# Kernel tuning notes

Measured on AMD Instinct MI355X. Metric: run time of the kernel, lower is better.

Reference implementation:

```python
import jax, jax.numpy as jnp
import numpy as np

B, CIN, H, W = 16, 1, 256, 256
WIDTH = 64
MODES = 32
LAYERS = 4
COUT = 1


def conv1x1(x, w, b):
    # x: [B,Ci,H,W], w: [Co,Ci], b: [Co]
    return jnp.einsum('bixy,oi->boxy', x, w) + b[None, :, None, None]


def mlp(x, w1, b1, w2, b2):
    # Conv2d(ci,mid,1) -> GELU(exact) -> Conv2d(mid,co,1)
    return conv1x1(jax.nn.gelu(conv1x1(x, w1, b1), approximate=False), w2, b2)


def spectral_conv2d(x, w1r, w1i, w2r, w2i):
    # x: [B,C,H,W]; weights: [Ci,Co,m1,m2] (real/imag parts of cfloat params)
    b, c, h, w = x.shape
    m1, m2 = w1r.shape[2], w1r.shape[3]
    co = w1r.shape[1]
    x_ft = jnp.fft.rfft2(x)  # [B,C,H,W//2+1] complex64
    w1 = w1r + 1j * w1i
    w2 = w2r + 1j * w2i
    top = jnp.einsum('bixy,ioxy->boxy', x_ft[:, :, :m1, :m2], w1)
    bot = jnp.einsum('bixy,ioxy->boxy', x_ft[:, :, -m1:, :m2], w2)
    out_ft = jnp.zeros((b, co, h, w // 2 + 1), dtype=x_ft.dtype)
    out_ft = out_ft.at[:, :, :m1, :m2].set(top).at[:, :, -m1:, :m2].set(bot)
    return jnp.fft.irfft2(out_ft, s=(h, w))


def setup_inputs() -> dict:
    key = jax.random.key(0)
    ks = iter(jax.random.split(key, 32))
    scale = 1.0 / (WIDTH * WIDTH)
    f32 = jnp.float32
    inp = {}
    inp['x'] = jax.random.normal(next(ks), (B, CIN, H, W), dtype=f32)
    # lifting 1x1 conv
    inp['p_w'] = jax.random.normal(next(ks), (WIDTH, CIN), dtype=f32) / np.sqrt(CIN)
    inp['p_b'] = jnp.zeros((WIDTH,), dtype=f32)
    # per-layer spectral weights (real/imag of uniform cfloat init)
    shp = (LAYERS, WIDTH, WIDTH, MODES, MODES)
    inp['sw1r'] = scale * jax.random.uniform(next(ks), shp, dtype=f32)
    inp['sw1i'] = scale * jax.random.uniform(next(ks), shp, dtype=f32)
    inp['sw2r'] = scale * jax.random.uniform(next(ks), shp, dtype=f32)
    inp['sw2i'] = scale * jax.random.uniform(next(ks), shp, dtype=f32)
    # per-layer channel MLP (mid_channels = WIDTH)
    inp['m1w'] = jax.random.normal(next(ks), (LAYERS, WIDTH, WIDTH), dtype=f32) / np.sqrt(WIDTH)
    inp['m1b'] = jnp.zeros((LAYERS, WIDTH), dtype=f32)
    inp['m2w'] = jax.random.normal(next(ks), (LAYERS, WIDTH, WIDTH), dtype=f32) / np.sqrt(WIDTH)
    inp['m2b'] = jnp.zeros((LAYERS, WIDTH), dtype=f32)
    # per-layer skip 1x1 conv
    inp['skw'] = jax.random.normal(next(ks), (LAYERS, WIDTH, WIDTH), dtype=f32) / np.sqrt(WIDTH)
    inp['skb'] = jnp.zeros((LAYERS, WIDTH), dtype=f32)
    # projection MLP (mid = 4*WIDTH)
    inp['q1w'] = jax.random.normal(next(ks), (4 * WIDTH, WIDTH), dtype=f32) / np.sqrt(WIDTH)
    inp['q1b'] = jnp.zeros((4 * WIDTH,), dtype=f32)
    inp['q2w'] = jax.random.normal(next(ks), (COUT, 4 * WIDTH), dtype=f32) / np.sqrt(4 * WIDTH)
    inp['q2b'] = jnp.zeros((COUT,), dtype=f32)
    return inp


def reference(x, p_w, p_b, sw1r, sw1i, sw2r, sw2i, m1w, m1b, m2w, m2b,
              skw, skb, q1w, q1b, q2w, q2b):
    h = conv1x1(x, p_w, p_b)  # lift to [B,WIDTH,H,W]
    for l in range(LAYERS):
        x1 = spectral_conv2d(h, sw1r[l], sw1i[l], sw2r[l], sw2i[l])
        x1 = mlp(x1, m1w[l], m1b[l], m2w[l], m2b[l])
        x2 = conv1x1(h, skw[l], skb[l])
        h = x1 + x2
        if l < LAYERS - 1:
            h = jax.nn.gelu(h, approximate=False)
    return mlp(h, q1w, q1b, q2w, q2b)  # [B,COUT,H,W]
```

## Files before the change

### kernel.cpp

```cpp
#include <hip/hip_runtime.h>
#include <math.h>

#define NC 64
#define NH 256
#define NW 256
#define NM 32
#define NKY 64
#define HW 65536

typedef short bfrag __attribute__((ext_vector_type(8)));
typedef float facc  __attribute__((ext_vector_type(4)));
#define MFMA(a,b,c) __builtin_amdgcn_mfma_f32_16x16x32_bf16(a,b,c,0,0,0)

static constexpr float PI_F = 3.14159265358979323846f;

__device__ __forceinline__ unsigned short f2b(float f) {
  unsigned b = __float_as_uint(f);
  return (unsigned short)((b + 0x7FFFu + ((b >> 16) & 1u)) >> 16);
}
__device__ __forceinline__ float b2f(unsigned short h) {
  return __uint_as_float((unsigned)h << 16);
}

__device__ __forceinline__ float gelu_f(float x) {
  float z = fabsf(x) * 0.70710678118654752f;
  float t = 1.0f / (1.0f + 0.3275911f * z);
  float e = __expf(-z * z);
  float p = t * (0.254829592f + t * (-0.284496736f + t * (1.421413741f +
            t * (-1.453152027f + t * 1.061405429f))));
  float er = copysignf(1.0f - p * e, x);
  return 0.5f * x * (1.0f + er);
}

__global__ void k_tEy(unsigned short* __restrict__ eh, unsigned short* __restrict__ el) {
  int i = blockIdx.x * 256 + threadIdx.x;
  int m = i >> 8, y = i & 255;
  int kyi = m & 63;
  int ky = (kyi < 32) ? kyi : (192 + kyi);
  int a = (ky * y) & 255;
  float s, c; sincosf((float)a * (PI_F / 128.f), &s, &c);
  float v = (m < 64) ? c : -s;
  unsigned short h = f2b(v);
  eh[i] = h; el[i] = f2b(v - b2f(h));
}
__global__ void k_tEx(unsigned short* __restrict__ eh, unsigned short* __restrict__ el) {
  int i = blockIdx.x * 256 + threadIdx.x;
  int m = i >> 9, k = i & 511;
  int x = k & 255, plane = k >> 8, kx = m & 31;
  int a = (kx * x) & 255;
  float s, c; sincosf((float)a * (PI_F / 128.f), &s, &c);
  float v = (m < 32) ? (plane ? s : c) : (plane ? c : -s);
  unsigned short h = f2b(v);
  eh[i] = h; el[i] = f2b(v - b2f(h));
}
__global__ void k_tWy(unsigned short* __restrict__ eh, unsigned short* __restrict__ el) {
  int i = blockIdx.x * 256 + threadIdx.x;
  int row = i >> 7, k = i & 127;
  int y = row & 255, part = row >> 8;
  int kyi = k & 63, plane = k >> 6;
  int ky = (kyi < 32) ? kyi : (192 + kyi);
  int a = (ky * y) & 255;
  float s, c; sincosf((float)a * (PI_F / 128.f), &s, &c);
  float v = (part == 0) ? (plane ? -s : c) : (plane ? c : s);
  unsigned short h = f2b(v);
  eh[i] = h; el[i] = f2b(v - b2f(h));
}
__global__ void k_tCx(unsigned short* __restrict__ eh, unsigned short* __restrict__ el) {
  int i = blockIdx.x * 256 + threadIdx.x;
  int x = i >> 6, k = i & 63;
  int kx = k & 31, plane = k >> 5;
  float w = ((kx == 0) ? 1.0f : 2.0f) / 65536.0f;
  int a = (kx * x) & 255;
  float s, c; sincosf((float)a * (PI_F / 128.f), &s, &c);
  float v = plane ? (-w * s) : (w * c);
  unsigned short h = f2b(v);
  eh[i] = h; el[i] = f2b(v - b2f(h));
}

__global__ void k_cvt2(const float* __restrict__ src, unsigned short* __restrict__ hi,
                       unsigned short* __restrict__ lo, int n) {
  int i = blockIdx.x * 256 + threadIdx.x;
  if (i < n) {
    float v = src[i];
    unsigned short h = f2b(v);
    hi[i] = h;
    lo[i] = f2b(v - b2f(h));
  }
}

__global__ __launch_bounds__(256) void k_lift(const float* __restrict__ x,
                                              const float* __restrict__ pw,
                                              const float* __restrict__ pb,
                                              unsigned short* __restrict__ hh,
                                              unsigned short* __restrict__ hl) {
  int b = blockIdx.y;
  int yx = blockIdx.x * 256 + threadIdx.x;
  float v = x[(size_t)b * HW + yx];
  size_t o = (size_t)b * NC * HW + yx;
  for (int c = 0; c < NC; ++c) {
    float u = v * pw[c] + pb[c];
    unsigned short hi = f2b(u);
    hh[o + (size_t)c * HW] = hi;
    hl[o + (size_t)c * HW] = f2b(u - b2f(hi));
  }
}

__global__ __launch_bounds__(256) void k_fy2(const unsigned short* __restrict__ hh,
                                             const unsigned short* __restrict__ hl,
                                             const unsigned short* __restrict__ Ah,
                                             const unsigned short* __restrict__ Al,
                                             float* __restrict__ Xc, int Ncol) {
  int tid = threadIdx.x, wv = tid >> 6, ln = tid & 63, g16 = ln >> 4, l15 = ln & 15;
  int colbase = blockIdx.x * 128 + wv * 32;
  facc acc[8][2];
#pragma unroll
  for (int mf = 0; mf < 8; ++mf)
#pragma unroll
    for (int pf = 0; pf < 2; ++pf) acc[mf][pf] = (facc)0.f;
#pragma unroll 1
  for (int ks = 0; ks < 8; ++ks) {
    int kof = g16 * 8 + 32 * ks;
    bfrag bh[2], bl[2];
#pragma unroll
    for (int pf = 0; pf < 2; ++pf) {
      int col = colbase + pf * 16 + l15;
      size_t o = (size_t)(col >> 8) * HW + (col & 255) + (size_t)kof * 256;
#pragma unroll
      for (int j = 0; j < 8; ++j) {
        bh[pf][j] = (short)hh[o + j * 256];
        bl[pf][j] = (short)hl[o + j * 256];
      }
    }
#pragma unroll
    for (int mf = 0; mf < 8; ++mf) {
      int row = 16 * mf + l15;
      bfrag ah = *(const bfrag*)(Ah + row * 256 + kof);
      bfrag al = *(const bfrag*)(Al + row * 256 + kof);
#pragma unroll
      for (int pf = 0; pf < 2; ++pf) {
        acc[mf][pf] = MFMA(ah, bh[pf], acc[mf][pf]);
        acc[mf][pf] = MFMA(ah, bl[pf], acc[mf][pf]);
        acc[mf][pf] = MFMA(al, bh[pf], acc[mf][pf]);
      }
    }
  }
#pragma unroll
  for (int mf = 0; mf < 8; ++mf)
#pragma unroll
    for (int pf = 0; pf < 2; ++pf) {
      int col = colbase + pf * 16 + l15;
#pragma unroll
      for (int r = 0; r < 4; ++r)
        Xc[(size_t)(16 * mf + 4 * g16 + r) * Ncol + col] = acc[mf][pf][r];
    }
}

__global__ __launch_bounds__(256) void k_fx2(const float* __restrict__ Xc,
                                             const unsigned short* __restrict__ Ah,
                                             const unsigned short* __restrict__ Al,
                                             float* __restrict__ X2r,
                                             float* __restrict__ X2i, int NcXc) {
  int tid = threadIdx.x, wv = tid >> 6, ln = tid & 63, g16 = ln >> 4, l15 = ln & 15;
  int colbase = blockIdx.x * 64 + wv * 16;
  facc acc[4];
#pragma unroll
  for (int mf = 0; mf < 4; ++mf) acc[mf] = (facc)0.f;
#pragma unroll 1
  for (int ks = 0; ks < 16; ++ks) {
    int plane = ks >> 3;
    int x0 = (ks & 7) * 32 + g16 * 8;
    int kof = g16 * 8 + 32 * ks;
    bfrag bh, bl;
    {
      int col = colbase + l15;
      const float* p = Xc + (size_t)(plane * 64 + (col & 63)) * NcXc + (col >> 6) * 256 + x0;
      float4 u0 = *(const float4*)p;
      float4 u1 = *(const float4*)(p + 4);
      float tv[8] = {u0.x, u0.y, u0.z, u0.w, u1.x, u1.y, u1.z, u1.w};
#pragma unroll
      for (int j = 0; j < 8; ++j) {
        unsigned short hi = f2b(tv[j]);
        bh[j] = (short)hi;
        bl[j] = (short)f2b(tv[j] - b2f(hi));
      }
    }
#pragma unroll
    for (int mf = 0; mf < 4; ++mf) {
      int row = 16 * mf + l15;
      bfrag ah = *(const bfrag*)(Ah + row * 512 + kof);
      bfrag al = *(const bfrag*)(Al + row * 512 + kof);
      acc[mf] = MFMA(ah, bh, acc[mf]);
      acc[mf] = MFMA(ah, bl, acc[mf]);
      acc[mf] = MFMA(al, bh, acc[mf]);
    }
  }
#pragma unroll
  for (int mf = 0; mf < 4; ++mf) {
    int col = colbase + l15;
    float* base = (mf >= 2) ? X2i : X2r;
    int kxb = 16 * (mf & 1) + 4 * g16;
    float4 v = make_float4(acc[mf][0], acc[mf][1], acc[mf][2], acc[mf][3]);
    *(float4*)(base + (size_t)col * 32 + kxb) = v;
  }
}

__global__ __launch_bounds__(512) void k_spec(const float* __restrict__ X2r,
                                              const float* __restrict__ X2i,
                                              const float* __restrict__ w1r,
                                              const float* __restrict__ w1i,
                                              const float* __restrict__ w2r,
                                              const float* __restrict__ w2i,
                                              float* __restrict__ S, int Ncs) {
  int b = blockIdx.y;
  int och = blockIdx.x & 3;
  int kyi = blockIdx.x >> 2;
  __shared__ float2 xs[NC * NM];
  for (int idx = threadIdx.x; idx < NC * NM; idx += 512) {
    int i = idx >> 5, kx = idx & 31;
    size_t c2 = ((size_t)(b * 64 + i) * 64 + kyi) * 32 + kx;
    xs[idx] = make_float2(X2r[c2], X2i[c2]);
  }
  __syncthreads();
  int kx = threadIdx.x & 31;
  int ol = threadIdx.x >> 5;
  int o = och * 16 + ol;
  int kym = kyi & 31;
  const float* wr = (kyi < 32) ? w1r : w2r;
  const float* wi = (kyi < 32) ? w1i : w2i;
  size_t wb = ((size_t)o * NM + kym) * NM + kx;
  float ar = 0.f, ai = 0.f;
#pragma unroll 4
  for (int i = 0; i < NC; ++i) {
    float2 xv = xs[i * NM + kx];
    float wrv = wr[wb + (size_t)i * 65536];
    float wiv = wi[wb + (size_t)i * 65536];
    ar += xv.x * wrv - xv.y * wiv;
    ai += xv.x * wiv + xv.y * wrv;
  }
  size_t cco = (size_t)(b * 64 + o) * 32 + kx;
  S[(size_t)kyi * Ncs + cco] = ar;
  S[(size_t)(64 + kyi) * Ncs + cco] = ai;
}

__global__ __launch_bounds__(256) void k_iy2(const float* __restrict__ S,
                                             const unsigned short* __restrict__ Ah,
                                             const unsigned short* __restrict__ Al,
                                             float* __restrict__ t2, int Ncs) {
  int tid = threadIdx.x, wv = tid >> 6, ln = tid & 63, g16 = ln >> 4, l15 = ln & 15;
  int colbase = blockIdx.x * 128 + wv * 32;
  int rowb = blockIdx.y * 64;
  facc acc[4][2];
#pragma unroll
  for (int mf = 0; mf < 4; ++mf)
#pragma unroll
    for (int pf = 0; pf < 2; ++pf) acc[mf][pf] = (facc)0.f;
#pragma unroll 1
  for (int ks = 0; ks < 4; ++ks) {
    int kof = g16 * 8 + 32 * ks;
    bfrag bh[2], bl[2];
#pragma unroll
    for (int pf = 0; pf < 2; ++pf) {
      int col = colbase + pf * 16 + l15;
      const float* p = S + (size_t)kof * Ncs + col;
#pragma unroll
      for (int j = 0; j < 8; ++j) {
        float v = p[(size_t)j * Ncs];
        unsigned short hi = f2b(v);
        bh[pf][j] = (short)hi;
        bl[pf][j] = (short)f2b(v - b2f(hi));
      }
    }
#pragma unroll
    for (int mf = 0; mf < 4; ++mf) {
      int row = rowb + 16 * mf + l15;
      bfrag ah = *(const bfrag*)(Ah + row * 128 + kof);
      bfrag al = *(const bfrag*)(Al + row * 128 + kof);
#pragma unroll
      for (int pf = 0; pf < 2; ++pf) {
        acc[mf][pf] = MFMA(ah, bh[pf], acc[mf][pf]);
        acc[mf][pf] = MFMA(ah, bl[pf], acc[mf][pf]);
        acc[mf][pf] = MFMA(al, bh[pf], acc[mf][pf]);
      }
    }
  }
#pragma unroll
  for (int mf = 0; mf < 4; ++mf)
#pragma unroll
    for (int pf = 0; pf < 2; ++pf) {
      int col = colbase + pf * 16 + l15;
#pragma unroll
      for (int r = 0; r < 4; ++r)
        t2[(size_t)(rowb + 16 * mf + 4 * g16 + r) * Ncs + col] = acc[mf][pf][r];
    }
}

__global__ __launch_bounds__(256) void k_ix2(const float* __restrict__ t2,
                                             const unsigned short* __restrict__ Ah,
                                             const unsigned short* __restrict__ Al,
                                             unsigned short* __restrict__ x1h,
                                             unsigned short* __restrict__ x1l, int Nct) {
  int tid = threadIdx.x, wv = tid >> 6, ln = tid & 63, g16 = ln >> 4, l15 = ln & 15;
  int colbase = blockIdx.x * 128 + wv * 32;
  int rowb = blockIdx.y * 128;
  facc acc[8][2];
#pragma unroll
  for (int mf = 0; mf < 8; ++mf)
#pragma unroll
    for (int pf = 0; pf < 2; ++pf) acc[mf][pf] = (facc)0.f;
#pragma unroll 1
  for (int ks = 0; ks < 2; ++ks) {
    int kof = g16 * 8 + 32 * ks;
    bfrag bh[2], bl[2];
#pragma unroll
    for (int pf = 0; pf < 2; ++pf) {
      int col = colbase + pf * 16 + l15;
      const float* p = t2 + (size_t)(ks * 256 + (col & 255)) * Nct + (col >> 8) * 32 + g16 * 8;
      float4 u0 = *(const float4*)p;
      float4 u1 = *(const float4*)(p + 4);
      float tv[8] = {u0.x, u0.y, u0.z, u0.w, u1.x, u1.y, u1.z, u1.w};
#pragma unroll
      for (int j = 0; j < 8; ++j) {
        unsigned short hi = f2b(tv[j]);
        bh[pf][j] = (short)hi;
        bl[pf][j] = (short)f2b(tv[j] - b2f(hi));
      }
    }
#pragma unroll
    for (int mf = 0; mf < 8; ++mf) {
      int row = rowb + 16 * mf + l15;
      bfrag ah = *(const bfrag*)(Ah + row * 64 + kof);
      bfrag al = *(const bfrag*)(Al + row * 64 + kof);
#pragma unroll
      for (int pf = 0; pf < 2; ++pf) {
        acc[mf][pf] = MFMA(ah, bh[pf], acc[mf][pf]);
        acc[mf][pf] = MFMA(ah, bl[pf], acc[mf][pf]);
        acc[mf][pf] = MFMA(al, bh[pf], acc[mf][pf]);
      }
    }
  }
#pragma unroll
  for (int mf = 0; mf < 8; ++mf)
#pragma unroll
    for (int pf = 0; pf < 2; ++pf) {
      int col = colbase + pf * 16 + l15;
      int bc = col >> 8, y = col & 255;
      int xb = rowb + 16 * mf + 4 * g16;
      ushort4 hv, lv;
#pragma unroll
      for (int r = 0; r < 4; ++r) {
        float v = acc[mf][pf][r];
        unsigned short hi = f2b(v);
        ((unsigned short*)&hv)[r] = hi;
        ((unsigned short*)&lv)[r] = f2b(v - b2f(hi));
      }
      size_t o = (size_t)bc * HW + y * 256 + xb;
      *(ushort4*)(x1h + o) = hv;
      *(ushort4*)(x1l + o) = lv;
    }
}

__global__ __launch_bounds__(256) void k_mlp1s(unsigned short* __restrict__ x1h,
                                               unsigned short* __restrict__ x1l,
                                               const unsigned short* __restrict__ w1h,
                                               const unsigned short* __restrict__ w1l,
                                               const float* __restrict__ b1p) {
  __shared__ unsigned short whs[64 * 72], wls[64 * 72];
  int tid = threadIdx.x;
  for (int i = tid; i < 64 * 64; i += 256) {
    int r = i >> 6, c = i & 63;
    whs[r * 72 + c] = w1h[i];
    wls[r * 72 + c] = w1l[i];
  }
  int wv = tid >> 6, ln = tid & 63, g16 = ln >> 4, l15 = ln & 15;
  int b = blockIdx.y;
  unsigned short* xh = x1h + (size_t)b * NC * HW;
  unsigned short* xl = x1l + (size_t)b * NC * HW;
  float b1v[4][4];
#pragma unroll
  for (int mf = 0; mf < 4; ++mf)
#pragma unroll
    for (int r = 0; r < 4; ++r) b1v[mf][r] = b1p[16 * mf + 4 * g16 + r];
  __syncthreads();
  for (int t = 0; t < 4; ++t) {
    int pxb = (blockIdx.x * 4 + t) * 128 + wv * 32;
    facc a1[4][2];
#pragma unroll
    for (int mf = 0; mf < 4; ++mf)
#pragma unroll
      for (int pf = 0; pf < 2; ++pf) {
        facc z; z[0] = b1v[mf][0]; z[1] = b1v[mf][1]; z[2] = b1v[mf][2]; z[3] = b1v[mf][3];
        a1[mf][pf] = z;
      }
#pragma unroll
    for (int ks = 0; ks < 2; ++ks) {
      bfrag xhb[2], xlb[2];
#pragma unroll
      for (int pf = 0; pf < 2; ++pf) {
        int px = pxb + pf * 16 + l15;
#pragma unroll
        for (int j = 0; j < 8; ++j) {
          int c = g16 * 8 + j + 32 * ks;
          xhb[pf][j] = (short)xh[(size_t)c * HW + px];
          xlb[pf][j] = (short)xl[(size_t)c * HW + px];
        }
      }
#pragma unroll
      for (int mf = 0; mf < 4; ++mf) {
        bfrag wh = *(const bfrag*)(whs + (16 * mf + l15) * 72 + g16 * 8 + 32 * ks);
        bfrag wl = *(const bfrag*)(wls + (16 * mf + l15) * 72 + g16 * 8 + 32 * ks);
#pragma unroll
        for (int pf = 0; pf < 2; ++pf) {
          a1[mf][pf] = MFMA(wh, xhb[pf], a1[mf][pf]);
          a1[mf][pf] = MFMA(wh, xlb[pf], a1[mf][pf]);
          a1[mf][pf] = MFMA(wl, xhb[pf], a1[mf][pf]);
        }
      }
    }
#pragma unroll
    for (int mf = 0; mf < 4; ++mf)
#pragma unroll
      for (int pf = 0; pf < 2; ++pf) {
        int px = pxb + pf * 16 + l15;
#pragma unroll
        for (int r = 0; r < 4; ++r) {
          float v = gelu_f(a1[mf][pf][r]);
          unsigned short hi = f2b(v);
          size_t idx = (size_t)(16 * mf + 4 * g16 + r) * HW + px;
          xh[idx] = hi;
          xl[idx] = f2b(v - b2f(hi));
        }
      }
  }
}

__global__ __launch_bounds__(256) void k_mix2(const unsigned short* __restrict__ midh,
                                              const unsigned short* __restrict__ midl,
                                              unsigned short* __restrict__ hh_,
                                              unsigned short* __restrict__ hl_,
                                              const unsigned short* __restrict__ w2h,
                                              const unsigned short* __restrict__ w2l,
                                              const unsigned short* __restrict__ skh,
                                              const unsigned short* __restrict__ skl,
                                              const float* __restrict__ b2p,
                                              const float* __restrict__ skbp,
                                              int do_gelu) {
  __shared__ unsigned short w2hs[64 * 72], w2ls[64 * 72], skhs[64 * 72], skls[64 * 72];
  int tid = threadIdx.x;
  for (int i = tid; i < 64 * 64; i += 256) {
    int r = i >> 6, c = i & 63;
    w2hs[r * 72 + c] = w2h[i];
    w2ls[r * 72 + c] = w2l[i];
    skhs[r * 72 + c] = skh[i];
    skls[r * 72 + c] = skl[i];
  }
  int wv = tid >> 6, ln = tid & 63, g16 = ln >> 4, l15 = ln & 15;
  int b = blockIdx.y;
  const unsigned short* mh = midh + (size_t)b * NC * HW;
  const unsigned short* ml = midl + (size_t)b * NC * HW;
  unsigned short* hbh = hh_ + (size_t)b * NC * HW;
  unsigned short* hbl = hl_ + (size_t)b * NC * HW;
  float b2v[4][4];
#pragma unroll
  for (int mf = 0; mf < 4; ++mf)
#pragma unroll
    for (int r = 0; r < 4; ++r) {
      int o = 16 * mf + 4 * g16 + r;
      b2v[mf][r] = b2p[o] + skbp[o];
    }
  __syncthreads();
  for (int t = 0; t < 4; ++t) {
    int pxb = (blockIdx.x * 4 + t) * 128 + wv * 32;
    facc a2[4][2];
#pragma unroll
    for (int mf = 0; mf < 4; ++mf)
#pragma unroll
      for (int pf = 0; pf < 2; ++pf) {
        facc z; z[0] = b2v[mf][0]; z[1] = b2v[mf][1]; z[2] = b2v[mf][2]; z[3] = b2v[mf][3];
        a2[mf][pf] = z;
      }
#pragma unroll
    for (int ks = 0; ks < 2; ++ks) {
      bfrag mhb[2], mlb[2], hhb[2], hlb[2];
#pragma unroll
      for (int pf = 0; pf < 2; ++pf) {
        int px = pxb + pf * 16 + l15;
#pragma unroll
        for (int j = 0; j < 8; ++j) {
          int c = g16 * 8 + j + 32 * ks;
          mhb[pf][j] = (short)mh[(size_t)c * HW + px];
          mlb[pf][j] = (short)ml[(size_t)c * HW + px];
          hhb[pf][j] = (short)hbh[(size_t)c * HW + px];
          hlb[pf][j] = (short)hbl[(size_t)c * HW + px];
        }
      }
#pragma unroll
      for (int mf = 0; mf < 4; ++mf) {
        bfrag w2hf = *(const bfrag*)(w2hs + (16 * mf + l15) * 72 + g16 * 8 + 32 * ks);
        bfrag w2lf = *(const bfrag*)(w2ls + (16 * mf + l15) * 72 + g16 * 8 + 32 * ks);
        bfrag skhf = *(const bfrag*)(skhs + (16 * mf + l15) * 72 + g16 * 8 + 32 * ks);
        bfrag sklf = *(const bfrag*)(skls + (16 * mf + l15) * 72 + g16 * 8 + 32 * ks);
#pragma unroll
        for (int pf = 0; pf < 2; ++pf) {
          a2[mf][pf] = MFMA(w2hf, mhb[pf], a2[mf][pf]);
          a2[mf][pf] = MFMA(w2hf, mlb[pf], a2[mf][pf]);
          a2[mf][pf] = MFMA(w2lf, mhb[pf], a2[mf][pf]);
          a2[mf][pf] = MFMA(skhf, hhb[pf], a2[mf][pf]);
          a2[mf][pf] = MFMA(skhf, hlb[pf], a2[mf][pf]);
          a2[mf][pf] = MFMA(sklf, hhb[pf], a2[mf][pf]);
        }
      }
    }
#pragma unroll
    for (int mf = 0; mf < 4; ++mf)
#pragma unroll
      for (int pf = 0; pf < 2; ++pf) {
        facc v = a2[mf][pf];
        if (do_gelu) {
          v[0] = gelu_f(v[0]); v[1] = gelu_f(v[1]);
          v[2] = gelu_f(v[2]); v[3] = gelu_f(v[3]);
        }
        int px = pxb + pf * 16 + l15;
#pragma unroll
        for (int r = 0; r < 4; ++r) {
          float u = v[r];
          unsigned short hi = f2b(u);
          size_t idx = (size_t)(16 * mf + 4 * g16 + r) * HW + px;
          hbh[idx] = hi;
          hbl[idx] = f2b(u - b2f(hi));
        }
      }
  }
}

__global__ __launch_bounds__(256) void k_proj3(const unsigned short* __restrict__ hh,
                                               const unsigned short* __restrict__ hl,
                                               const unsigned short* __restrict__ q1h,
                                               const unsigned short* __restrict__ q1l,
                                               const float* __restrict__ q1bp,
                                               const float* __restrict__ q2wp,
                                               const float* __restrict__ q2bp,
                                               float* __restrict__ out) {
  __shared__ unsigned short q1sh[256 * 72];
  __shared__ unsigned short q1sl[256 * 72];
  int tid = threadIdx.x;
  for (int i = tid; i < 256 * 64; i += 256) {
    int r = i >> 6, c = i & 63;
    q1sh[r * 72 + c] = q1h[i];
    q1sl[r * 72 + c] = q1l[i];
  }
  int wv = tid >> 6, ln = tid & 63, g16 = ln >> 4, l15 = ln & 15;
  int b = blockIdx.y;
  const unsigned short* hbh = hh + (size_t)b * NC * HW;
  const unsigned short* hbl = hl + (size_t)b * NC * HW;
  float bq[16][4], qv[16][4];
#pragma unroll
  for (int mf = 0; mf < 16; ++mf)
#pragma unroll
    for (int r = 0; r < 4; ++r) {
      int row = 16 * mf + 4 * g16 + r;
      bq[mf][r] = q1bp[row];
      qv[mf][r] = q2wp[row];
    }
  float q2bias = q2bp[0];
  __syncthreads();
  for (int t = 0; t < 4; ++t) {
    int px0 = blockIdx.x * 256 + t * 64 + wv * 16;
    bfrag hhb[2], hlb[2];
#pragma unroll
    for (int ks = 0; ks < 2; ++ks)
#pragma unroll
      for (int j = 0; j < 8; ++j) {
        int c = g16 * 8 + j + 32 * ks;
        hhb[ks][j] = (short)hbh[(size_t)c * HW + px0 + l15];
        hlb[ks][j] = (short)hbl[(size_t)c * HW + px0 + l15];
      }
    float partial = 0.f;
#pragma unroll
    for (int mf = 0; mf < 16; ++mf) {
      facc acc;
      acc[0] = bq[mf][0]; acc[1] = bq[mf][1]; acc[2] = bq[mf][2]; acc[3] = bq[mf][3];
#pragma unroll
      for (int ks = 0; ks < 2; ++ks) {
        bfrag ah = *(const bfrag*)(q1sh + (16 * mf + l15) * 72 + g16 * 8 + 32 * ks);
        bfrag al = *(const bfrag*)(q1sl + (16 * mf + l15) * 72 + g16 * 8 + 32 * ks);
        acc = MFMA(ah, hhb[ks], acc);
        acc = MFMA(ah, hlb[ks], acc);
        acc = MFMA(al, hhb[ks], acc);
      }
#pragma unroll
      for (int r = 0; r < 4; ++r)
        partial += gelu_f(acc[r]) * qv[mf][r];
    }
    partial += __shfl_xor(partial, 16);
    partial += __shfl_xor(partial, 32);
    if (ln < 16)
      out[(size_t)b * HW + px0 + ln] = partial + q2bias;
  }
}

extern "C" void kernel_launch(void* const* d_in, const int* in_sizes, int n_in,
                              void* d_out, int out_size, void* d_ws, size_t ws_size,
                              hipStream_t stream) {
  const float* x    = (const float*)d_in[0];
  const float* p_w  = (const float*)d_in[1];
  const float* p_b  = (const float*)d_in[2];
  const float* sw1r = (const float*)d_in[3];
  const float* sw1i = (const float*)d_in[4];
  const float* sw2r = (const float*)d_in[5];
  const float* sw2i = (const float*)d_in[6];
  const float* m1w  = (const float*)d_in[7];
  const float* m1b  = (const float*)d_in[8];
  const float* m2w  = (const float*)d_in[9];
  const float* m2b  = (const float*)d_in[10];
  const float* skw  = (const float*)d_in[11];
  const float* skb  = (const float*)d_in[12];
  const float* q1w  = (const float*)d_in[13];
  const float* q1b  = (const float*)d_in[14];
  const float* q2w  = (const float*)d_in[15];
  const float* q2b  = (const float*)d_in[16];

  const size_t MB = 1048576ULL;
  const size_t TBL = 1 * MB;
  int g = 16;
  while (g > 1 && (size_t)g * 36 * MB + TBL > ws_size) g >>= 1;
  if ((size_t)g * 36 * MB + TBL > ws_size) return;

  char* wsb = (char*)d_ws;
  unsigned short* Eyh = (unsigned short*)(wsb + 0);
  unsigned short* Eyl = (unsigned short*)(wsb + 65536);
  unsigned short* Exh = (unsigned short*)(wsb + 131072);
  unsigned short* Exl = (unsigned short*)(wsb + 196608);
  unsigned short* Wyh = (unsigned short*)(wsb + 262144);
  unsigned short* Wyl = (unsigned short*)(wsb + 393216);
  unsigned short* Cxh = (unsigned short*)(wsb + 524288);
  unsigned short* Cxl = (unsigned short*)(wsb + 557056);
  unsigned short* m1h = (unsigned short*)(wsb + 589824);
  unsigned short* m1l = (unsigned short*)(wsb + 622592);
  unsigned short* m2h = (unsigned short*)(wsb + 655360);
  unsigned short* m2l = (unsigned short*)(wsb + 688128);
  unsigned short* skh = (unsigned short*)(wsb + 720896);
  unsigned short* skl = (unsigned short*)(wsb + 753664);
  unsigned short* q1h = (unsigned short*)(wsb + 786432);
  unsigned short* q1l = (unsigned short*)(wsb + 819200);

  char* base = wsb + TBL;
  unsigned short* Hh = (unsigned short*)base;
  unsigned short* Hl = (unsigned short*)(base + (size_t)g * 8 * MB);
  unsigned short* x1h = (unsigned short*)(base + (size_t)g * 16 * MB);
  unsigned short* x1l = (unsigned short*)(base + (size_t)g * 24 * MB);
  float* Xc  = (float*)x1h;
  float* X2r = (float*)x1l;
  float* X2i = (float*)((char*)x1l + (size_t)g * 512 * 1024);
  float* S   = (float*)((char*)x1l + (size_t)g * 1 * MB);
  float* t2  = (float*)(base + (size_t)g * 32 * MB);

  k_tEy<<<128, 256, 0, stream>>>(Eyh, Eyl);
  k_tEx<<<128, 256, 0, stream>>>(Exh, Exl);
  k_tWy<<<256, 256, 0, stream>>>(Wyh, Wyl);
  k_tCx<<<64, 256, 0, stream>>>(Cxh, Cxl);
  k_cvt2<<<64, 256, 0, stream>>>(m1w, m1h, m1l, 16384);
  k_cvt2<<<64, 256, 0, stream>>>(m2w, m2h, m2l, 16384);
  k_cvt2<<<64, 256, 0, stream>>>(skw, skh, skl, 16384);
  k_cvt2<<<64, 256, 0, stream>>>(q1w, q1h, q1l, 16384);

  int Nfy = g * 16384;
  int Ncs = g * 2048;

  for (int b0 = 0; b0 < 16; b0 += g) {
    k_lift<<<dim3(256, g), 256, 0, stream>>>(x + (size_t)b0 * HW, p_w, p_b, Hh, Hl);
    for (int l = 0; l < 4; ++l) {
      k_fy2<<<g * 128, 256, 0, stream>>>(Hh, Hl, Eyh, Eyl, Xc, Nfy);
      k_fx2<<<g * 64, 256, 0, stream>>>(Xc, Exh, Exl, X2r, X2i, Nfy);
      k_spec<<<dim3(256, g), 512, 0, stream>>>(X2r, X2i,
                                               sw1r + (size_t)l * 4194304,
                                               sw1i + (size_t)l * 4194304,
                                               sw2r + (size_t)l * 4194304,
                                               sw2i + (size_t)l * 4194304, S, Ncs);
      k_iy2<<<dim3(g * 16, 8), 256, 0, stream>>>(S, Wyh, Wyl, t2, Ncs);
      k_ix2<<<dim3(g * 128, 2), 256, 0, stream>>>(t2, Cxh, Cxl, x1h, x1l, Ncs);
      k_mlp1s<<<dim3(128, g), 256, 0, stream>>>(x1h, x1l, m1h + l * 4096, m1l + l * 4096,
                                                m1b + l * 64);
      k_mix2<<<dim3(128, g), 256, 0, stream>>>(x1h, x1l, Hh, Hl, m2h + l * 4096, m2l + l * 4096,
                                               skh + l * 4096, skl + l * 4096,
                                               m2b + l * 64, skb + l * 64, (l < 3) ? 1 : 0);
    }
    k_proj3<<<dim3(256, g), 256, 0, stream>>>(Hh, Hl, q1h, q1l, q1b, q2w, q2b,
                                              (float*)d_out + (size_t)b0 * HW);
  }
}
```

Measured before the change: 4.252 ms.

## Split projection MLP into two half-row passes with register-blocked MFMA tiles

Measured after the change: 4.245 ms. Within noise of the previous version (-0.2%).

```diff
diff --git a/kernel.cpp b/kernel.cpp
--- a/kernel.cpp
+++ b/kernel.cpp
@@ -532,69 +532,86 @@
   }
 }
 
-__global__ __launch_bounds__(256) void k_proj3(const unsigned short* __restrict__ hh,
+__global__ __launch_bounds__(256) void k_pproj(const unsigned short* __restrict__ hh,
                                                const unsigned short* __restrict__ hl,
                                                const unsigned short* __restrict__ q1h,
                                                const unsigned short* __restrict__ q1l,
                                                const float* __restrict__ q1bp,
                                                const float* __restrict__ q2wp,
                                                const float* __restrict__ q2bp,
-                                               float* __restrict__ out) {
-  __shared__ unsigned short q1sh[256 * 72];
-  __shared__ unsigned short q1sl[256 * 72];
+                                               float* __restrict__ out,
+                                               int R0, int accum) {
+  __shared__ unsigned short q1sh[128 * 72];
+  __shared__ unsigned short q1sl[128 * 72];
+  __shared__ float q1bs[128], q2s[128];
   int tid = threadIdx.x;
-  for (int i = tid; i < 256 * 64; i += 256) {
-    int r = i >> 6, c = i & 63;
-    q1sh[r * 72 + c] = q1h[i];
-    q1sl[r * 72 + c] = q1l[i];
+  for (int i = tid; i < 2048; i += 256) {
+    int row = i >> 4, c4 = (i & 15) * 4;
+    ushort4 vh = *(const ushort4*)(q1h + (size_t)(R0 + row) * 64 + c4);
+    ushort4 vl = *(const ushort4*)(q1l + (size_t)(R0 + row) * 64 + c4);
+    *(ushort4*)(q1sh + row * 72 + c4) = vh;
+    *(ushort4*)(q1sl + row * 72 + c4) = vl;
+  }
+  if (tid < 128) {
+    q1bs[tid] = q1bp[R0 + tid];
+    q2s[tid] = q2wp[R0 + tid];
   }
   int wv = tid >> 6, ln = tid & 63, g16 = ln >> 4, l15 = ln & 15;
-  int b = blockIdx.y;
-  const unsigned short* hbh = hh + (size_t)b * NC * HW;
-  const unsigned short* hbl = hl + (size_t)b * NC * HW;
-  float bq[16][4], qv[16][4];
-#pragma unroll
-  for (int mf = 0; mf < 16; ++mf)
-#pragma unroll
-    for (int r = 0; r < 4; ++r) {
-      int row = 16 * mf + 4 * g16 + r;
-      bq[mf][r] = q1bp[row];
-      qv[mf][r] = q2wp[row];
-    }
   float q2bias = q2bp[0];
   __syncthreads();
-  for (int t = 0; t < 4; ++t) {
-    int px0 = blockIdx.x * 256 + t * 64 + wv * 16;
-    bfrag hhb[2], hlb[2];
-#pragma unroll
-    for (int ks = 0; ks < 2; ++ks)
+
+  int colbase = blockIdx.x * 128 + wv * 32;
+  facc acc[8][2];
+#pragma unroll
+  for (int mf = 0; mf < 8; ++mf)
+#pragma unroll
+    for (int pf = 0; pf < 2; ++pf) {
+      facc z;
+#pragma unroll
+      for (int r = 0; r < 4; ++r) z[r] = q1bs[16 * mf + 4 * g16 + r];
+      acc[mf][pf] = z;
+    }
+#pragma unroll
+  for (int ks = 0; ks < 2; ++ks) {
+    bfrag bh[2], bl[2];
+#pragma unroll
+    for (int pf = 0; pf < 2; ++pf) {
+      int col = colbase + pf * 16 + l15;
+      size_t o = (size_t)(col >> 16) * NC * HW + (col & 65535);
 #pragma unroll
       for (int j = 0; j < 8; ++j) {
         int c = g16 * 8 + j + 32 * ks;
-        hhb[ks][j] = (short)hbh[(size_t)c * HW + px0 + l15];
-        hlb[ks][j] = (short)hbl[(size_t)c * HW + px0 + l15];
-      }
+        bh[pf][j] = (short)hh[o + (size_t)c * HW];
+        bl[pf][j] = (short)hl[o + (size_t)c * HW];
+      }
+    }
+#pragma unroll
+    for (int mf = 0; mf < 8; ++mf) {
+      bfrag ah = *(const bfrag*)(q1sh + (16 * mf + l15) * 72 + g16 * 8 + 32 * ks);
+      bfrag al = *(const bfrag*)(q1sl + (16 * mf + l15) * 72 + g16 * 8 + 32 * ks);
+#pragma unroll
+      for (int pf = 0; pf < 2; ++pf) {
+        acc[mf][pf] = MFMA(ah, bh[pf], acc[mf][pf]);
+        acc[mf][pf] = MFMA(ah, bl[pf], acc[mf][pf]);
+        acc[mf][pf] = MFMA(al, bh[pf], acc[mf][pf]);
+      }
+    }
+  }
+#pragma unroll
+  for (int pf = 0; pf < 2; ++pf) {
     float partial = 0.f;
 #pragma unroll
-    for (int mf = 0; mf < 16; ++mf) {
-      facc acc;
-      acc[0] = bq[mf][0]; acc[1] = bq[mf][1]; acc[2] = bq[mf][2]; acc[3] = bq[mf][3];
-#pragma unroll
-      for (int ks = 0; ks < 2; ++ks) {
-        bfrag ah = *(const bfrag*)(q1sh + (16 * mf + l15) * 72 + g16 * 8 + 32 * ks);
-        bfrag al = *(const bfrag*)(q1sl + (16 * mf + l15) * 72 + g16 * 8 + 32 * ks);
-        acc = MFMA(ah, hhb[ks], acc);
-        acc = MFMA(ah, hlb[ks], acc);
-        acc = MFMA(al, hhb[ks], acc);
-      }
+    for (int mf = 0; mf < 8; ++mf)
 #pragma unroll
       for (int r = 0; r < 4; ++r)
-        partial += gelu_f(acc[r]) * qv[mf][r];
-    }
+        partial += gelu_f(acc[mf][pf][r]) * q2s[16 * mf + 4 * g16 + r];
     partial += __shfl_xor(partial, 16);
     partial += __shfl_xor(partial, 32);
-    if (ln < 16)
-      out[(size_t)b * HW + px0 + ln] = partial + q2bias;
+    if (ln < 16) {
+      int col = colbase + pf * 16 + ln;
+      if (accum) out[col] += partial;
+      else out[col] = partial + q2bias;
+    }
   }
 }
 
@@ -684,7 +701,8 @@
                                                skh + l * 4096, skl + l * 4096,
                                                m2b + l * 64, skb + l * 64, (l < 3) ? 1 : 0);
     }
-    k_proj3<<<dim3(256, g), 256, 0, stream>>>(Hh, Hl, q1h, q1l, q1b, q2w, q2b,
-                                              (float*)d_out + (size_t)b0 * HW);
-  }
-}
+    float* outc = (float*)d_out + (size_t)b0 * HW;
+    k_pproj<<<g * 512, 256, 0, stream>>>(Hh, Hl, q1h, q1l, q1b, q2w, q2b, outc, 0, 0);
+    k_pproj<<<g * 512, 256, 0, stream>>>(Hh, Hl, q1h, q1l, q1b, q2w, q2b, outc, 128, 1);
+  }
+}
```
